# Kernel optimization log

Measured on AMD Instinct MI355X. Metric: run time of the kernel, lower is better.

Reference implementation:

```python
import jax, jax.numpy as jnp
import numpy as np

B, T, D = 2, 2048, 2048
NH, NKV, HD = 16, 4, 128
EPS = 1e-6
SCALE = HD ** -0.5


def setup_inputs() -> dict:
    key = jax.random.key(0)
    ks = jax.random.split(key, 6)
    hidden = jax.random.normal(ks[0], (B, T, D), dtype=jnp.float32)
    # realistic RoPE tables: [B, T, HD], freqs repeated over both halves
    pos = jnp.arange(T, dtype=jnp.float32)
    inv_freq = 1.0 / (10000.0 ** (jnp.arange(0, HD, 2, dtype=jnp.float32) / HD))
    freqs = pos[:, None] * inv_freq[None, :]            # [T, HD/2]
    emb = jnp.concatenate([freqs, freqs], axis=-1)      # [T, HD]
    cos = jnp.broadcast_to(jnp.cos(emb)[None], (B, T, HD))
    sin = jnp.broadcast_to(jnp.sin(emb)[None], (B, T, HD))
    s = 0.02
    return {
        "hidden_BTD": hidden,
        "cos_BTK": cos,
        "sin_BTK": sin,
        "segment_ids_BT": jnp.zeros((B, T), dtype=jnp.int32),
        "position_ids_BT": jnp.broadcast_to(jnp.arange(T, dtype=jnp.int32)[None], (B, T)),
        "w_q": jax.random.normal(ks[1], (D, NH * HD * 2), dtype=jnp.float32) * s,
        "w_k": jax.random.normal(ks[2], (D, NKV * HD), dtype=jnp.float32) * s,
        "w_v": jax.random.normal(ks[3], (D, NKV * HD), dtype=jnp.float32) * s,
        "w_o": jax.random.normal(ks[4], (NH * HD, D), dtype=jnp.float32) * s,
        "q_norm_w": jnp.ones((HD,), dtype=jnp.float32),
        "k_norm_w": jnp.ones((HD,), dtype=jnp.float32),
    }


def _rms_norm(x, w):
    var = jnp.mean(jnp.square(x), axis=-1, keepdims=True)
    return x * jax.lax.rsqrt(var + EPS) * w


def _rotate_half(x):
    x1, x2 = jnp.split(x, 2, axis=-1)
    return jnp.concatenate([-x2, x1], axis=-1)


def _apply_rope(x, cos, sin):
    # x: [B,T,H,K]; cos/sin: [B,T,K] broadcast over heads
    c = cos[:, :, None, :]
    s = sin[:, :, None, :]
    return x * c + _rotate_half(x) * s


def reference(hidden_BTD, cos_BTK, sin_BTK, segment_ids_BT, position_ids_BT,
              w_q, w_k, w_v, w_o, q_norm_w, k_norm_w):
    Bn, Tn, _ = hidden_BTD.shape
    n_rep = NH // NKV
    # fused Q + gate projection, then split
    q_out = (hidden_BTD @ w_q).reshape(Bn, Tn, NH, HD * 2)
    q, gate = jnp.split(q_out, 2, axis=-1)                  # [B,T,H,K] each
    gate_BTD = gate.reshape(Bn, Tn, NH * HD)
    q = _rms_norm(q, q_norm_w)
    k = _rms_norm((hidden_BTD @ w_k).reshape(Bn, Tn, NKV, HD), k_norm_w)
    v = (hidden_BTD @ w_v).reshape(Bn, Tn, NKV, HD)
    q = _apply_rope(q, cos_BTK, sin_BTK)
    k = _apply_rope(k, cos_BTK, sin_BTK)
    # GQA: repeat kv heads
    k = jnp.repeat(k, n_rep, axis=2)                        # [B,T,H,K]
    v = jnp.repeat(v, n_rep, axis=2)
    scores = jnp.einsum('bqhk,bkhd->bhqd'.replace('d', 'K').replace('K', 'k') if False else 'bihk,bjhk->bhij', q, k) * SCALE
    causal = jnp.tril(jnp.ones((Tn, Tn), dtype=bool))
    scores = jnp.where(causal[None, None], scores, jnp.finfo(scores.dtype).min)
    probs = jax.nn.softmax(scores, axis=-1)
    attn = jnp.einsum('bhij,bjhk->bihk', probs, v)          # [B,T,H,K]
    attn_BTD = attn.reshape(Bn, Tn, NH * HD)
    attn_BTD = attn_BTD * jax.nn.sigmoid(gate_BTD)
    return attn_BTD @ w_o
```

## Files before the change

### kernel.cpp

```cpp
#include <hip/hip_runtime.h>
#include <hip/hip_bf16.h>

#define DEVI __device__ __forceinline__

typedef __attribute__((ext_vector_type(4))) float f32x4;
typedef __attribute__((ext_vector_type(8))) short s16x8;
typedef __attribute__((ext_vector_type(4))) short s16x4;

static constexpr int B_   = 2;
static constexpr int T_   = 2048;
static constexpr int D_   = 2048;
static constexpr int NH_  = 16;
static constexpr int NKV_ = 4;
static constexpr int HD_  = 128;
static constexpr int M_   = B_ * T_;
static constexpr int NQK  = NH_ * HD_ * 2;
static constexpr int NKC  = NKV_ * HD_;
static constexpr int NTOT = NQK + 2 * NKC;
static constexpr float SCALE_ = 0.08838834764831845f;

DEVI short f2bf(float f) {
    __hip_bfloat16 h = __float2bfloat16(f);
    return __builtin_bit_cast(short, h);
}
DEVI float bf2f(short s) {
    unsigned int u = ((unsigned int)(unsigned short)s) << 16;
    return __builtin_bit_cast(float, u);
}
DEVI void store_out(short* p, float v) { *p = f2bf(v); }
DEVI void store_out(float* p, float v) { *p = v; }

DEVI f32x4 mfma16(s16x8 a, s16x8 b, f32x4 c) {
    return __builtin_amdgcn_mfma_f32_16x16x32_bf16(a, b, c, 0, 0, 0);
}

DEVI void gload_lds16(const void* g, void* l) {
    __builtin_amdgcn_global_load_lds(
        (const __attribute__((address_space(1))) void*)g,
        (__attribute__((address_space(3))) void*)l,
        16, 0, 0);
}

__global__ void cast_f32_bf16(const float* __restrict__ in, short* __restrict__ out) {
    int i = (blockIdx.x * 256 + threadIdx.x) << 2;
    f32x4 v = *(const f32x4*)(in + i);
    s16x4 o;
#pragma unroll
    for (int j = 0; j < 4; ++j) o[j] = f2bf(v[j]);
    *(s16x4*)(out + i) = o;
}

__global__ void transpose_cast(const float* __restrict__ src, short* __restrict__ dst,
                               int R, int C) {
    __shared__ float tile[32][33];
    int c0 = blockIdx.x << 5, r0 = blockIdx.y << 5;
    int tx = threadIdx.x, ty = threadIdx.y;
#pragma unroll
    for (int i = 0; i < 32; i += 8)
        tile[ty + i][tx] = src[(long)(r0 + ty + i) * C + c0 + tx];
    __syncthreads();
#pragma unroll
    for (int i = 0; i < 32; i += 8)
        dst[(long)(c0 + ty + i) * R + r0 + tx] = f2bf(tile[tx][ty + i]);
}

template <typename OUT>
__global__ __launch_bounds__(256, 2) void gemm_bf16(
    const short* __restrict__ A, const short* __restrict__ Bt,
    OUT* __restrict__ C, int M, int N, int K) {
    __shared__ __align__(16) short Asm[2][128 * 32];
    __shared__ __align__(16) short Bsm[2][128 * 32];
    int tid = threadIdx.x;
    int nbx = N >> 7;
    int bx = blockIdx.x % nbx, by = blockIdx.x / nbx;
    int row0 = by << 7, col0 = bx << 7;
    int lane = tid & 63, wave = tid >> 6;
    int wr = (wave >> 1) << 6, wc = (wave & 1) << 6;
    int g = lane >> 4, rl = lane & 15;
    int srow = tid >> 2, scol = (tid & 3) << 3;
    const short* Ag = A + (long)(row0 + srow) * K + scol;
    const short* Bg = Bt + (long)(col0 + srow) * K + scol;

    f32x4 acc[4][4];
#pragma unroll
    for (int i = 0; i < 4; ++i)
#pragma unroll
        for (int j = 0; j < 4; ++j) acc[i][j] = f32x4{0.f, 0.f, 0.f, 0.f};

    auto stage = [&](int buf, int kt) {
        int ko = kt << 5;
        gload_lds16(Ag + ko,            &Asm[buf][tid * 8]);
        gload_lds16(Ag + (K << 6) + ko, &Asm[buf][(tid + 256) * 8]);
        gload_lds16(Bg + ko,            &Bsm[buf][tid * 8]);
        gload_lds16(Bg + (K << 6) + ko, &Bsm[buf][(tid + 256) * 8]);
    };

    int KT = K >> 5;
    stage(0, 0);
    for (int kt = 0; kt < KT; ++kt) {
        __syncthreads();
        int buf = kt & 1;
        if (kt + 1 < KT) stage(buf ^ 1, kt + 1);
        const short* As = &Asm[buf][0];
        const short* Bs = &Bsm[buf][0];
        s16x8 af[4], bfr[4];
#pragma unroll
        for (int i = 0; i < 4; ++i) {
            af[i]  = *(const s16x8*)(As + (wr + i * 16 + rl) * 32 + g * 8);
            bfr[i] = *(const s16x8*)(Bs + (wc + i * 16 + rl) * 32 + g * 8);
        }
#pragma unroll
        for (int i = 0; i < 4; ++i)
#pragma unroll
            for (int j = 0; j < 4; ++j)
                acc[i][j] = mfma16(af[i], bfr[j], acc[i][j]);
    }
#pragma unroll
    for (int i = 0; i < 4; ++i)
#pragma unroll
        for (int j = 0; j < 4; ++j)
#pragma unroll
            for (int r = 0; r < 4; ++r) {
                int row = row0 + wr + i * 16 + 4 * g + r;
                int col = col0 + wc + j * 16 + rl;
                store_out(&C[(long)row * N + col], acc[i][j][r]);
            }
}

__global__ void postproc(const short* __restrict__ qkv, const float* __restrict__ cosp,
                         const float* __restrict__ sinp, const float* __restrict__ qw,
                         const float* __restrict__ kw, short* __restrict__ Q,
                         short* __restrict__ K) {
    int task = blockIdx.x * 4 + (threadIdx.x >> 6);
    int lane = threadIdx.x & 63;
    int bt = task / 20, sub = task - bt * 20;
    int b = bt >> 11, t = bt & (T_ - 1);
    bool isq = sub < 16;
    int h = isq ? sub : sub - 16;
    const short* src = qkv + (long)bt * NTOT + (isq ? h * 256 : NQK + h * HD_);
    const float* w = isq ? qw : kw;
    float x0 = bf2f(src[lane]);
    float x1 = bf2f(src[lane + 64]);
    float ss = x0 * x0 + x1 * x1;
    ss += __shfl_xor(ss, 32); ss += __shfl_xor(ss, 16); ss += __shfl_xor(ss, 8);
    ss += __shfl_xor(ss, 4);  ss += __shfl_xor(ss, 2);  ss += __shfl_xor(ss, 1);
    float rn = rsqrtf(ss * (1.0f / 128.0f) + 1e-6f);
    x0 *= rn * w[lane];
    x1 *= rn * w[lane + 64];
    float c0 = cosp[bt * HD_ + lane], c1 = cosp[bt * HD_ + lane + 64];
    float s0 = sinp[bt * HD_ + lane], s1 = sinp[bt * HD_ + lane + 64];
    float y0 = x0 * c0 - x1 * s0;
    float y1 = x1 * c1 + x0 * s1;
    short* dst;
    if (isq) {
        y0 *= SCALE_; y1 *= SCALE_;
        dst = Q + ((long)(b * NH_ + h) * T_ + t) * HD_;
    } else {
        dst = K + ((long)(b * NKV_ + h) * T_ + t) * HD_;
    }
    dst[lane]      = f2bf(y0);
    dst[lane + 64] = f2bf(y1);
}

__global__ void transpose_v(const short* __restrict__ qkv, short* __restrict__ VT) {
    __shared__ short tile[32][33];
    int bh = blockIdx.z;
    int b = bh >> 2, h = bh & 3;
    int t0 = blockIdx.x << 5, d0 = blockIdx.y << 5;
    int tx = threadIdx.x, ty = threadIdx.y;
    const short* src = qkv + (long)b * T_ * NTOT + NQK + NKC + h * HD_;
#pragma unroll
    for (int i = 0; i < 32; i += 8)
        tile[ty + i][tx] = src[(long)(t0 + ty + i) * NTOT + d0 + tx];
    __syncthreads();
    short* dst = VT + ((long)(b * NKV_ + h) * HD_ + d0) * T_ + t0;
#pragma unroll
    for (int i = 0; i < 32; i += 8)
        dst[(long)(ty + i) * T_ + tx] = tile[tx][ty + i];
}

__global__ __launch_bounds__(256) void fattn(
    const short* __restrict__ Q, const short* __restrict__ K,
    const short* __restrict__ VT, const short* __restrict__ qkv,
    short* __restrict__ AG) {
    __shared__ __align__(16) short Pl[4][16 * 32];
    int idx = blockIdx.x;
    int qt = idx & 31;
    int h = (idx >> 5) & 15;
    int b = idx >> 9;
    int lane = threadIdx.x & 63, wave = threadIdx.x >> 6;
    int qbase = qt * 64 + wave * 16;
    int kvh = h >> 2;
    const short* Qp = Q + ((long)(b * NH_ + h) * T_ + qbase) * HD_;
    const short* Kp = K + (long)(b * NKV_ + kvh) * T_ * HD_;
    const short* Vp = VT + (long)(b * NKV_ + kvh) * HD_ * T_;
    int g = lane >> 4, rl = lane & 15;

    s16x8 qf[4];
#pragma unroll
    for (int c = 0; c < 4; ++c)
        qf[c] = *(const s16x8*)(Qp + rl * HD_ + c * 32 + g * 8);

    f32x4 o[8];
#pragma unroll
    for (int dt = 0; dt < 8; ++dt) o[dt] = f32x4{0.f, 0.f, 0.f, 0.f};
    float m[4] = {-1e30f, -1e30f, -1e30f, -1e30f};
    float l[4] = {0.f, 0.f, 0.f, 0.f};
    short* Pw = &Pl[wave][0];

    int ntiles = (qbase + 47) >> 5;
    for (int kt = 0; kt < ntiles; ++kt) {
        int k0 = kt * 32;
        f32x4 s0 = {0.f, 0.f, 0.f, 0.f}, s1 = {0.f, 0.f, 0.f, 0.f};
#pragma unroll
        for (int c = 0; c < 4; ++c) {
            s16x8 kf0 = *(const s16x8*)(Kp + (long)(k0 + rl) * HD_ + c * 32 + g * 8);
            s16x8 kf1 = *(const s16x8*)(Kp + (long)(k0 + 16 + rl) * HD_ + c * 32 + g * 8);
            s0 = mfma16(qf[c], kf0, s0);
            s1 = mfma16(qf[c], kf1, s1);
        }
        if (k0 + 31 > qbase) {
#pragma unroll
            for (int r = 0; r < 4; ++r) {
                int qi = qbase + 4 * g + r;
                if (k0 + rl > qi)      s0[r] = -1e30f;
                if (k0 + 16 + rl > qi) s1[r] = -1e30f;
            }
        }
        float fr[4];
#pragma unroll
        for (int r = 0; r < 4; ++r) {
            float v = fmaxf(s0[r], s1[r]);
            v = fmaxf(v, __shfl_xor(v, 1));
            v = fmaxf(v, __shfl_xor(v, 2));
            v = fmaxf(v, __shfl_xor(v, 4));
            v = fmaxf(v, __shfl_xor(v, 8));
            float mn = fmaxf(m[r], v);
            fr[r] = __expf(m[r] - mn);
            m[r] = mn;
            s0[r] = __expf(s0[r] - mn);
            s1[r] = __expf(s1[r] - mn);
            float rs = s0[r] + s1[r];
            rs += __shfl_xor(rs, 1); rs += __shfl_xor(rs, 2);
            rs += __shfl_xor(rs, 4); rs += __shfl_xor(rs, 8);
            l[r] = l[r] * fr[r] + rs;
        }
        f32x4 fv = {fr[0], fr[1], fr[2], fr[3]};
#pragma unroll
        for (int dt = 0; dt < 8; ++dt) o[dt] *= fv;
#pragma unroll
        for (int r = 0; r < 4; ++r) {
            int row = 4 * g + r;
            int sw = (row & 3) << 3;
            Pw[(row * 32 + rl) ^ sw]      = f2bf(s0[r]);
            Pw[(row * 32 + 16 + rl) ^ sw] = f2bf(s1[r]);
        }
        s16x8 pa = *(const s16x8*)(Pw + rl * 32 + ((g ^ (rl & 3)) << 3));
#pragma unroll
        for (int dt = 0; dt < 8; ++dt) {
            s16x8 vf = *(const s16x8*)(Vp + (long)(dt * 16 + rl) * T_ + k0 + g * 8);
            o[dt] = mfma16(pa, vf, o[dt]);
        }
    }
#pragma unroll
    for (int r = 0; r < 4; ++r) {
        int qi = qbase + 4 * g + r;
        long btr = (long)b * T_ + qi;
        float inv = 1.0f / l[r];
#pragma unroll
        for (int dt = 0; dt < 8; ++dt) {
            int d = dt * 16 + rl;
            float gate = bf2f(qkv[btr * NTOT + h * 256 + 128 + d]);
            float gv = 1.0f / (1.0f + __expf(-gate));
            AG[btr * (NH_ * HD_) + h * HD_ + d] = f2bf(o[dt][r] * inv * gv);
        }
    }
}

extern "C" void kernel_launch(void* const* d_in, const int* in_sizes, int n_in,
                              void* d_out, int out_size, void* d_ws, size_t ws_size,
                              hipStream_t stream) {
    (void)in_sizes; (void)n_in; (void)out_size; (void)ws_size;
    const float* hidden = (const float*)d_in[0];
    const float* cosp   = (const float*)d_in[1];
    const float* sinp   = (const float*)d_in[2];
    const float* w_q    = (const float*)d_in[5];
    const float* w_k    = (const float*)d_in[6];
    const float* w_v    = (const float*)d_in[7];
    const float* w_o    = (const float*)d_in[8];
    const float* qnw    = (const float*)d_in[9];
    const float* knw    = (const float*)d_in[10];

    short* ws      = (short*)d_ws;
    short* hiddenb = ws;
    short* wqkvT   = hiddenb + (long)M_ * D_;
    short* woT     = wqkvT + (long)NTOT * D_;
    short* qkvb    = woT + (long)D_ * D_;
    short* Qb      = qkvb + (long)M_ * NTOT;
    short* Kb      = Qb + (long)B_ * NH_ * T_ * HD_;
    short* VTb     = Kb + (long)B_ * NKV_ * T_ * HD_;
    short* AGb     = VTb + (long)B_ * NKV_ * T_ * HD_;
    float* out     = (float*)d_out;

    dim3 tblk(32, 8);
    cast_f32_bf16<<<(M_ * D_) / 1024, 256, 0, stream>>>(hidden, hiddenb);
    transpose_cast<<<dim3(NQK / 32, D_ / 32), tblk, 0, stream>>>(w_q, wqkvT, D_, NQK);
    transpose_cast<<<dim3(NKC / 32, D_ / 32), tblk, 0, stream>>>(w_k, wqkvT + (long)NQK * D_, D_, NKC);
    transpose_cast<<<dim3(NKC / 32, D_ / 32), tblk, 0, stream>>>(w_v, wqkvT + (long)(NQK + NKC) * D_, D_, NKC);
    transpose_cast<<<dim3(D_ / 32, D_ / 32), tblk, 0, stream>>>(w_o, woT, D_, D_);

    gemm_bf16<short><<<(M_ / 128) * (NTOT / 128), 256, 0, stream>>>(
        hiddenb, wqkvT, qkvb, M_, NTOT, D_);

    postproc<<<(M_ * 20) / 4, 256, 0, stream>>>(qkvb, cosp, sinp, qnw, knw, Qb, Kb);
    transpose_v<<<dim3(T_ / 32, HD_ / 32, B_ * NKV_), tblk, 0, stream>>>(qkvb, VTb);

    fattn<<<B_ * NH_ * (T_ / 64), 256, 0, stream>>>(Qb, Kb, VTb, qkvb, AGb);

    gemm_bf16<float><<<(M_ / 128) * (D_ / 128), 256, 0, stream>>>(
        AGb, woT, out, M_, D_, D_);
}
```

Baseline: 781.1 us.

## Pair causal query tiles per wave and compute transposed scores to skip LDS

```diff
diff --git a/kernel.cpp b/kernel.cpp
--- a/kernel.cpp
+++ b/kernel.cpp
@@ -179,102 +179,129 @@
         dst[(long)(ty + i) * T_ + tx] = tile[tx][ty + i];
 }
 
+DEVI void softstep(f32x4& s0, f32x4& s1, float& m, float& l, f32x4 o[8],
+                   s16x8& pa, int k0, int qb, int g, int rl) {
+    if (k0 + 31 > qb) {
+        int q = qb + rl;
+#pragma unroll
+        for (int r = 0; r < 4; ++r) {
+            if (k0 + 4 * g + r > q)      s0[r] = -1e30f;
+            if (k0 + 16 + 4 * g + r > q) s1[r] = -1e30f;
+        }
+    }
+    float tm = fmaxf(fmaxf(fmaxf(s0[0], s0[1]), fmaxf(s0[2], s0[3])),
+                     fmaxf(fmaxf(s1[0], s1[1]), fmaxf(s1[2], s1[3])));
+    tm = fmaxf(tm, __shfl_xor(tm, 16));
+    tm = fmaxf(tm, __shfl_xor(tm, 32));
+    float mn = fmaxf(m, tm);
+    float fr = __expf(m - mn);
+    m = mn;
+    float p[8];
+#pragma unroll
+    for (int r = 0; r < 4; ++r) {
+        p[r]     = __expf(s0[r] - mn);
+        p[4 + r] = __expf(s1[r] - mn);
+    }
+    float rs = ((p[0] + p[1]) + (p[2] + p[3])) + ((p[4] + p[5]) + (p[6] + p[7]));
+    rs += __shfl_xor(rs, 16);
+    rs += __shfl_xor(rs, 32);
+    l = l * fr + rs;
+    f32x4 fq;
+#pragma unroll
+    for (int r = 0; r < 4; ++r) fq[r] = __shfl(fr, 4 * g + r);
+#pragma unroll
+    for (int dt = 0; dt < 8; ++dt) o[dt] *= fq;
+    s16x8 t;
+#pragma unroll
+    for (int i = 0; i < 8; ++i) t[i] = f2bf(p[i]);
+    pa = t;
+}
+
+DEVI void epilogue(const f32x4 o[8], float l, int qb, int b, int h, int g, int rl,
+                   const short* __restrict__ qkv, short* __restrict__ AG) {
+    f32x4 linv;
+#pragma unroll
+    for (int r = 0; r < 4; ++r) linv[r] = 1.0f / __shfl(l, 4 * g + r);
+#pragma unroll
+    for (int r = 0; r < 4; ++r) {
+        int qi = qb + 4 * g + r;
+        long btr = (long)b * T_ + qi;
+#pragma unroll
+        for (int dt = 0; dt < 8; ++dt) {
+            int d = dt * 16 + rl;
+            float gate = bf2f(qkv[btr * NTOT + h * 256 + 128 + d]);
+            float gv = 1.0f / (1.0f + __expf(-gate));
+            AG[btr * (NH_ * HD_) + h * HD_ + d] = f2bf(o[dt][r] * linv[r] * gv);
+        }
+    }
+}
+
 __global__ __launch_bounds__(256) void fattn(
     const short* __restrict__ Q, const short* __restrict__ K,
     const short* __restrict__ VT, const short* __restrict__ qkv,
     short* __restrict__ AG) {
-    __shared__ __align__(16) short Pl[4][16 * 32];
-    int idx = blockIdx.x;
-    int qt = idx & 31;
-    int h = (idx >> 5) & 15;
-    int b = idx >> 9;
-    int lane = threadIdx.x & 63, wave = threadIdx.x >> 6;
-    int qbase = qt * 64 + wave * 16;
+    int wid  = blockIdx.x * 4 + (threadIdx.x >> 6);
+    int lane = threadIdx.x & 63;
+    int g = lane >> 4, rl = lane & 15;
+    int j = wid & 63;
+    int h = (wid >> 6) & 15;
+    int b = wid >> 10;
     int kvh = h >> 2;
-    const short* Qp = Q + ((long)(b * NH_ + h) * T_ + qbase) * HD_;
+    int qbA = j << 4;
+    int qbB = (127 - j) << 4;
+    const short* Qp = Q + (long)(b * NH_ + h) * T_ * HD_;
     const short* Kp = K + (long)(b * NKV_ + kvh) * T_ * HD_;
     const short* Vp = VT + (long)(b * NKV_ + kvh) * HD_ * T_;
-    int g = lane >> 4, rl = lane & 15;
-
-    s16x8 qf[4];
-#pragma unroll
-    for (int c = 0; c < 4; ++c)
-        qf[c] = *(const s16x8*)(Qp + rl * HD_ + c * 32 + g * 8);
-
-    f32x4 o[8];
-#pragma unroll
-    for (int dt = 0; dt < 8; ++dt) o[dt] = f32x4{0.f, 0.f, 0.f, 0.f};
-    float m[4] = {-1e30f, -1e30f, -1e30f, -1e30f};
-    float l[4] = {0.f, 0.f, 0.f, 0.f};
-    short* Pw = &Pl[wave][0];
-
-    int ntiles = (qbase + 47) >> 5;
-    for (int kt = 0; kt < ntiles; ++kt) {
-        int k0 = kt * 32;
-        f32x4 s0 = {0.f, 0.f, 0.f, 0.f}, s1 = {0.f, 0.f, 0.f, 0.f};
+
+    s16x8 qfA[4], qfB[4];
+#pragma unroll
+    for (int c = 0; c < 4; ++c) {
+        qfA[c] = *(const s16x8*)(Qp + (long)(qbA + rl) * HD_ + c * 32 + g * 8);
+        qfB[c] = *(const s16x8*)(Qp + (long)(qbB + rl) * HD_ + c * 32 + g * 8);
+    }
+
+    f32x4 oA[8], oB[8];
+#pragma unroll
+    for (int dt = 0; dt < 8; ++dt) {
+        oA[dt] = f32x4{0.f, 0.f, 0.f, 0.f};
+        oB[dt] = f32x4{0.f, 0.f, 0.f, 0.f};
+    }
+    float mA = -1e30f, lA = 0.f, mB = -1e30f, lB = 0.f;
+
+    int ntA = (qbA + 47) >> 5;
+    int ntB = (qbB + 47) >> 5;
+
+    for (int kt = 0; kt < ntB; ++kt) {
+        int k0 = kt << 5;
+        bool doA = kt < ntA;
+        f32x4 sA0 = {0.f, 0.f, 0.f, 0.f}, sA1 = {0.f, 0.f, 0.f, 0.f};
+        f32x4 sB0 = {0.f, 0.f, 0.f, 0.f}, sB1 = {0.f, 0.f, 0.f, 0.f};
 #pragma unroll
         for (int c = 0; c < 4; ++c) {
             s16x8 kf0 = *(const s16x8*)(Kp + (long)(k0 + rl) * HD_ + c * 32 + g * 8);
             s16x8 kf1 = *(const s16x8*)(Kp + (long)(k0 + 16 + rl) * HD_ + c * 32 + g * 8);
-            s0 = mfma16(qf[c], kf0, s0);
-            s1 = mfma16(qf[c], kf1, s1);
-        }
-        if (k0 + 31 > qbase) {
-#pragma unroll
-            for (int r = 0; r < 4; ++r) {
-                int qi = qbase + 4 * g + r;
-                if (k0 + rl > qi)      s0[r] = -1e30f;
-                if (k0 + 16 + rl > qi) s1[r] = -1e30f;
+            sB0 = mfma16(kf0, qfB[c], sB0);
+            sB1 = mfma16(kf1, qfB[c], sB1);
+            if (doA) {
+                sA0 = mfma16(kf0, qfA[c], sA0);
+                sA1 = mfma16(kf1, qfA[c], sA1);
             }
         }
-        float fr[4];
-#pragma unroll
-        for (int r = 0; r < 4; ++r) {
-            float v = fmaxf(s0[r], s1[r]);
-            v = fmaxf(v, __shfl_xor(v, 1));
-            v = fmaxf(v, __shfl_xor(v, 2));
-            v = fmaxf(v, __shfl_xor(v, 4));
-            v = fmaxf(v, __shfl_xor(v, 8));
-            float mn = fmaxf(m[r], v);
-            fr[r] = __expf(m[r] - mn);
-            m[r] = mn;
-            s0[r] = __expf(s0[r] - mn);
-            s1[r] = __expf(s1[r] - mn);
-            float rs = s0[r] + s1[r];
-            rs += __shfl_xor(rs, 1); rs += __shfl_xor(rs, 2);
-            rs += __shfl_xor(rs, 4); rs += __shfl_xor(rs, 8);
-            l[r] = l[r] * fr[r] + rs;
-        }
-        f32x4 fv = {fr[0], fr[1], fr[2], fr[3]};
-#pragma unroll
-        for (int dt = 0; dt < 8; ++dt) o[dt] *= fv;
-#pragma unroll
-        for (int r = 0; r < 4; ++r) {
-            int row = 4 * g + r;
-            int sw = (row & 3) << 3;
-            Pw[(row * 32 + rl) ^ sw]      = f2bf(s0[r]);
-            Pw[(row * 32 + 16 + rl) ^ sw] = f2bf(s1[r]);
-        }
-        s16x8 pa = *(const s16x8*)(Pw + rl * 32 + ((g ^ (rl & 3)) << 3));
+        s16x8 paA, paB;
+        softstep(sB0, sB1, mB, lB, oB, paB, k0, qbB, g, rl);
+        if (doA) softstep(sA0, sA1, mA, lA, oA, paA, k0, qbA, g, rl);
 #pragma unroll
         for (int dt = 0; dt < 8; ++dt) {
-            s16x8 vf = *(const s16x8*)(Vp + (long)(dt * 16 + rl) * T_ + k0 + g * 8);
-            o[dt] = mfma16(pa, vf, o[dt]);
-        }
-    }
-#pragma unroll
-    for (int r = 0; r < 4; ++r) {
-        int qi = qbase + 4 * g + r;
-        long btr = (long)b * T_ + qi;
-        float inv = 1.0f / l[r];
-#pragma unroll
-        for (int dt = 0; dt < 8; ++dt) {
-            int d = dt * 16 + rl;
-            float gate = bf2f(qkv[btr * NTOT + h * 256 + 128 + d]);
-            float gv = 1.0f / (1.0f + __expf(-gate));
-            AG[btr * (NH_ * HD_) + h * HD_ + d] = f2bf(o[dt][r] * inv * gv);
-        }
-    }
+            const short* vp = Vp + (long)(dt * 16 + rl) * T_ + k0 + 4 * g;
+            s16x4 v0 = *(const s16x4*)vp;
+            s16x4 v1 = *(const s16x4*)(vp + 16);
+            s16x8 vf = __builtin_shufflevector(v0, v1, 0, 1, 2, 3, 4, 5, 6, 7);
+            oB[dt] = mfma16(paB, vf, oB[dt]);
+            if (doA) oA[dt] = mfma16(paA, vf, oA[dt]);
+        }
+    }
+    epilogue(oB, lB, qbB, b, h, g, rl, qkv, AG);
+    epilogue(oA, lA, qbA, b, h, g, rl, qkv, AG);
 }
 
 extern "C" void kernel_launch(void* const* d_in, const int* in_sizes, int n_in,
@@ -315,7 +342,7 @@
     postproc<<<(M_ * 20) / 4, 256, 0, stream>>>(qkvb, cosp, sinp, qnw, knw, Qb, Kb);
     transpose_v<<<dim3(T_ / 32, HD_ / 32, B_ * NKV_), tblk, 0, stream>>>(qkvb, VTb);
 
-    fattn<<<B_ * NH_ * (T_ / 64), 256, 0, stream>>>(Qb, Kb, VTb, qkvb, AGb);
+    fattn<<<512, 256, 0, stream>>>(Qb, Kb, VTb, qkvb, AGb);
 
     gemm_bf16<float><<<(M_ / 128) * (D_ / 128), 256, 0, stream>>>(
         AGb, woT, out, M_, D_, D_);
```

Measured after the change: 673.3 us. -13.8%, faster.
